# Kernel tuning notes

Hardware: AMD Instinct MI355X
Metric: run time of the kernel (lower is better)

## Reference

```python
import jax, jax.numpy as jnp
import numpy as np

B, H, N, D, RPE = 2, 8, 4096, 64, 64
LAYERS = 3


def _rms(x):
    # SimpleRMSNorm: x / sqrt(mean(x^2) + eps), no learned scale
    return x / jnp.sqrt(jnp.mean(x * x, axis=-1, keepdims=True) + 1e-8)


def setup_inputs() -> dict:
    key = jax.random.key(0)
    ks = jax.random.split(key, 7)
    s = 1.0 / np.sqrt(RPE)
    return {
        "x": jax.random.normal(ks[0], (B, H, N, D), dtype=jnp.float32),
        "w_in": jax.random.normal(ks[1], (1, RPE), dtype=jnp.float32) * 0.5,
        "b_in": jax.random.normal(ks[2], (RPE,), dtype=jnp.float32) * 0.02,
        "w_hid": jax.random.normal(ks[3], (LAYERS, RPE, RPE), dtype=jnp.float32) * s,
        "b_hid": jax.random.normal(ks[4], (LAYERS, RPE), dtype=jnp.float32) * 0.02,
        "w_out": jax.random.normal(ks[5], (RPE, H * D), dtype=jnp.float32) * s,
        "b_out": jax.random.normal(ks[6], (H * D,), dtype=jnp.float32) * 0.02,
    }


def reference(x, w_in, b_in, w_hid, b_hid, w_out, b_out):
    n = x.shape[-2]
    dt = x.dtype

    def rpe(idx):  # idx: (m, 1) relative-position features
        h = idx @ w_in + b_in  # (m, RPE)
        for i in range(LAYERS):  # non-residual: x = layer(x)
            h = jax.nn.relu(_rms(h)) @ w_hid[i] + b_hid[i]
        h = jax.nn.relu(_rms(h)) @ w_out + b_out  # (m, H*D)
        return h.reshape(-1, H, D).transpose(1, 0, 2)  # (H, m, D)

    zero_idx = jnp.ones((1, 1), dt)
    pos_idx = (1.0 / jnp.arange(2, n + 1, dtype=dt)).reshape(n - 1, 1)
    neg_idx = (-1.0 / jnp.arange(n, 1, -1, dtype=dt)).reshape(n - 1, 1)

    zero_k = rpe(zero_idx)  # (H, 1, D); used for both T[0] slots like the torch code
    a = jnp.concatenate([zero_k, rpe(pos_idx), zero_k, rpe(neg_idx)], axis=1)  # (H, 2n, D)
    # act_type='none' -> identity activation on a

    # Toeplitz matvec as circular conv of length 2n via FFT
    y = jnp.fft.rfft(x, 2 * n, axis=-2)          # (B, H, n+1, D) complex
    v = jnp.fft.rfft(a, 2 * n, axis=-2)[None]    # (1, H, n+1, D) complex
    out = jnp.fft.irfft(v * y, 2 * n, axis=-2)[:, :, :n, :]
    return out.astype(dt)
```

## Files before the change

### kernel.cpp

```cpp
#include <hip/hip_runtime.h>

#define N_SEQ 4096
#define N_FFT 8192
#define LAYERS 3
#define FT 512
#define PIDX(i) ((i) + ((i) >> 5))

template<int M>
__device__ inline void pass16_fwd(float* re, float* im, int tid)
{
    const int Q = M >> 4;
    const int j = tid & (Q - 1);
    const int G = tid / Q;
    const int base = G * M + j;
    const float KR[4] = {1.f, 0.9238795325f, 0.7071067812f, 0.3826834324f};
    const float KI[4] = {0.f, -0.3826834324f, -0.7071067812f, -0.9238795325f};
    float xr[4][4], xi[4][4];
#pragma unroll
    for (int a = 0; a < 4; ++a)
#pragma unroll
        for (int b = 0; b < 4; ++b) {
            int idx = PIDX(base + a * (M >> 2) + b * Q);
            xr[a][b] = re[idx]; xi[a][b] = im[idx];
        }
    float cj, sj;
    __sincosf(-6.283185307179586f / (float)M * (float)j, &sj, &cj);
#pragma unroll
    for (int b = 0; b < 4; ++b) {
        float c1 = cj * KR[b] - sj * KI[b];
        float s1 = cj * KI[b] + sj * KR[b];
        float c2 = c1 * c1 - s1 * s1, s2 = 2.f * c1 * s1;
        float c3 = c2 * c1 - s2 * s1, s3 = c2 * s1 + s2 * c1;
        float ar = xr[0][b] + xr[2][b], ai = xi[0][b] + xi[2][b];
        float br = xr[0][b] - xr[2][b], bi = xi[0][b] - xi[2][b];
        float cr = xr[1][b] + xr[3][b], ci = xi[1][b] + xi[3][b];
        float dr = xi[1][b] - xi[3][b], di = -(xr[1][b] - xr[3][b]);
        xr[0][b] = ar + cr;               xi[0][b] = ai + ci;
        float t1r = br + dr, t1i = bi + di;
        xr[1][b] = t1r * c1 - t1i * s1;   xi[1][b] = t1r * s1 + t1i * c1;
        float t2r = ar - cr, t2i = ai - ci;
        xr[2][b] = t2r * c2 - t2i * s2;   xi[2][b] = t2r * s2 + t2i * c2;
        float t3r = br - dr, t3i = bi - di;
        xr[3][b] = t3r * c3 - t3i * s3;   xi[3][b] = t3r * s3 + t3i * c3;
    }
    {
        float e1c = cj * cj - sj * sj, e1s = 2.f * cj * sj;
        float c1 = e1c * e1c - e1s * e1s, s1 = 2.f * e1c * e1s;
        float c2 = c1 * c1 - s1 * s1, s2 = 2.f * c1 * s1;
        float c3 = c2 * c1 - s2 * s1, s3 = c2 * s1 + s2 * c1;
#pragma unroll
        for (int a = 0; a < 4; ++a) {
            float ar = xr[a][0] + xr[a][2], ai = xi[a][0] + xi[a][2];
            float br = xr[a][0] - xr[a][2], bi = xi[a][0] - xi[a][2];
            float cr = xr[a][1] + xr[a][3], ci = xi[a][1] + xi[a][3];
            float dr = xi[a][1] - xi[a][3], di = -(xr[a][1] - xr[a][3]);
            xr[a][0] = ar + cr;               xi[a][0] = ai + ci;
            float t1r = br + dr, t1i = bi + di;
            xr[a][1] = t1r * c1 - t1i * s1;   xi[a][1] = t1r * s1 + t1i * c1;
            float t2r = ar - cr, t2i = ai - ci;
            xr[a][2] = t2r * c2 - t2i * s2;   xi[a][2] = t2r * s2 + t2i * c2;
            float t3r = br - dr, t3i = bi - di;
            xr[a][3] = t3r * c3 - t3i * s3;   xi[a][3] = t3r * s3 + t3i * c3;
        }
    }
#pragma unroll
    for (int a = 0; a < 4; ++a)
#pragma unroll
        for (int b = 0; b < 4; ++b) {
            int idx = PIDX(base + a * (M >> 2) + b * Q);
            re[idx] = xr[a][b]; im[idx] = xi[a][b];
        }
}

template<int M>
__device__ inline void pass16_inv(float* re, float* im, int tid)
{
    const int Q = M >> 4;
    const int j = tid & (Q - 1);
    const int G = tid / Q;
    const int base = G * M + j;
    const float KR[4] = {1.f, 0.9238795325f, 0.7071067812f, 0.3826834324f};
    const float KI[4] = {0.f, 0.3826834324f, 0.7071067812f, 0.9238795325f};
    float xr[4][4], xi[4][4];
#pragma unroll
    for (int a = 0; a < 4; ++a)
#pragma unroll
        for (int b = 0; b < 4; ++b) {
            int idx = PIDX(base + a * (M >> 2) + b * Q);
            xr[a][b] = re[idx]; xi[a][b] = im[idx];
        }
    float cj, sj;
    __sincosf(6.283185307179586f / (float)M * (float)j, &sj, &cj);
    {
        float e1c = cj * cj - sj * sj, e1s = 2.f * cj * sj;
        float c1 = e1c * e1c - e1s * e1s, s1 = 2.f * e1c * e1s;
        float c2 = c1 * c1 - s1 * s1, s2 = 2.f * c1 * s1;
        float c3 = c2 * c1 - s2 * s1, s3 = c2 * s1 + s2 * c1;
#pragma unroll
        for (int a = 0; a < 4; ++a) {
            float t0r = xr[a][0], t0i = xi[a][0];
            float t1r = xr[a][1] * c1 - xi[a][1] * s1, t1i = xr[a][1] * s1 + xi[a][1] * c1;
            float t2r = xr[a][2] * c2 - xi[a][2] * s2, t2i = xr[a][2] * s2 + xi[a][2] * c2;
            float t3r = xr[a][3] * c3 - xi[a][3] * s3, t3i = xr[a][3] * s3 + xi[a][3] * c3;
            float pr = t0r + t2r, pi = t0i + t2i;
            float qr = t0r - t2r, qi = t0i - t2i;
            float rr = t1r + t3r, ri = t1i + t3i;
            float sr = -(t1i - t3i), si = t1r - t3r;
            xr[a][0] = pr + rr; xi[a][0] = pi + ri;
            xr[a][1] = qr + sr; xi[a][1] = qi + si;
            xr[a][2] = pr - rr; xi[a][2] = pi - ri;
            xr[a][3] = qr - sr; xi[a][3] = qi - si;
        }
    }
#pragma unroll
    for (int b = 0; b < 4; ++b) {
        float c1 = cj * KR[b] - sj * KI[b];
        float s1 = cj * KI[b] + sj * KR[b];
        float c2 = c1 * c1 - s1 * s1, s2 = 2.f * c1 * s1;
        float c3 = c2 * c1 - s2 * s1, s3 = c2 * s1 + s2 * c1;
        float t0r = xr[0][b], t0i = xi[0][b];
        float t1r = xr[1][b] * c1 - xi[1][b] * s1, t1i = xr[1][b] * s1 + xi[1][b] * c1;
        float t2r = xr[2][b] * c2 - xi[2][b] * s2, t2i = xr[2][b] * s2 + xi[2][b] * c2;
        float t3r = xr[3][b] * c3 - xi[3][b] * s3, t3i = xr[3][b] * s3 + xi[3][b] * c3;
        float pr = t0r + t2r, pi = t0i + t2i;
        float qr = t0r - t2r, qi = t0i - t2i;
        float rr = t1r + t3r, ri = t1i + t3i;
        float sr = -(t1i - t3i), si = t1r - t3r;
        xr[0][b] = pr + rr; xi[0][b] = pi + ri;
        xr[1][b] = qr + sr; xi[1][b] = qi + si;
        xr[2][b] = pr - rr; xi[2][b] = pi - ri;
        xr[3][b] = qr - sr; xi[3][b] = qi - si;
    }
#pragma unroll
    for (int a = 0; a < 4; ++a)
#pragma unroll
        for (int b = 0; b < 4; ++b) {
            int idx = PIDX(base + a * (M >> 2) + b * Q);
            re[idx] = xr[a][b]; im[idx] = xi[a][b];
        }
}

__device__ inline void fwd8(float* zr, float* zi, int o)
{
    const float R = 0.70710678118654752f;
    {
        float ar = zr[o] + zr[o+4], ai = zi[o] + zi[o+4];
        float br = zr[o] - zr[o+4], bi = zi[o] - zi[o+4];
        float cr = zr[o+2] + zr[o+6], ci = zi[o+2] + zi[o+6];
        float dr = zi[o+2] - zi[o+6], di = -(zr[o+2] - zr[o+6]);
        zr[o]   = ar + cr; zi[o]   = ai + ci;
        zr[o+2] = br + dr; zi[o+2] = bi + di;
        zr[o+4] = ar - cr; zi[o+4] = ai - ci;
        zr[o+6] = br - dr; zi[o+6] = bi - di;
    }
    {
        float ar = zr[o+1] + zr[o+5], ai = zi[o+1] + zi[o+5];
        float br = zr[o+1] - zr[o+5], bi = zi[o+1] - zi[o+5];
        float cr = zr[o+3] + zr[o+7], ci = zi[o+3] + zi[o+7];
        float dr = zi[o+3] - zi[o+7], di = -(zr[o+3] - zr[o+7]);
        zr[o+1] = ar + cr; zi[o+1] = ai + ci;
        float t1r = br + dr, t1i = bi + di;
        zr[o+3] = R * (t1r + t1i); zi[o+3] = R * (t1i - t1r);
        float t2r = ar - cr, t2i = ai - ci;
        zr[o+5] = t2i;  zi[o+5] = -t2r;
        float t3r = br - dr, t3i = bi - di;
        zr[o+7] = R * (t3i - t3r); zi[o+7] = -R * (t3r + t3i);
    }
#pragma unroll
    for (int p = 0; p < 8; p += 2) {
        float ur = zr[o+p], ui = zi[o+p], vr = zr[o+p+1], vi = zi[o+p+1];
        zr[o+p]   = ur + vr; zi[o+p]   = ui + vi;
        zr[o+p+1] = ur - vr; zi[o+p+1] = ui - vi;
    }
}

__device__ inline void inv8(float* zr, float* zi, int o)
{
    const float R = 0.70710678118654752f;
#pragma unroll
    for (int p = 0; p < 8; p += 2) {
        float ur = zr[o+p], ui = zi[o+p], vr = zr[o+p+1], vi = zi[o+p+1];
        zr[o+p]   = ur + vr; zi[o+p]   = ui + vi;
        zr[o+p+1] = ur - vr; zi[o+p+1] = ui - vi;
    }
    {
        float t0r = zr[o],   t0i = zi[o];
        float t1r = zr[o+2], t1i = zi[o+2];
        float t2r = zr[o+4], t2i = zi[o+4];
        float t3r = zr[o+6], t3i = zi[o+6];
        float pr = t0r + t2r, pi = t0i + t2i;
        float qr = t0r - t2r, qi = t0i - t2i;
        float rr = t1r + t3r, ri = t1i + t3i;
        float sr = -(t1i - t3i), si = t1r - t3r;
        zr[o]   = pr + rr; zi[o]   = pi + ri;
        zr[o+2] = qr + sr; zi[o+2] = qi + si;
        zr[o+4] = pr - rr; zi[o+4] = pi - ri;
        zr[o+6] = qr - sr; zi[o+6] = qi - si;
    }
    {
        float t0r = zr[o+1], t0i = zi[o+1];
        float yr = zr[o+3], yi = zi[o+3];
        float t1r = R * (yr - yi), t1i = R * (yr + yi);
        yr = zr[o+5]; yi = zi[o+5];
        float t2r = -yi, t2i = yr;
        yr = zr[o+7]; yi = zi[o+7];
        float t3r = -R * (yr + yi), t3i = R * (yr - yi);
        float pr = t0r + t2r, pi = t0i + t2i;
        float qr = t0r - t2r, qi = t0i - t2i;
        float rr = t1r + t3r, ri = t1i + t3i;
        float sr = -(t1i - t3i), si = t1r - t3r;
        zr[o+1] = pr + rr; zi[o+1] = pi + ri;
        zr[o+3] = qr + sr; zi[o+3] = qi + si;
        zr[o+5] = pr - rr; zi[o+5] = pi - ri;
        zr[o+7] = qr - sr; zi[o+7] = qi - si;
    }
}

__global__ __launch_bounds__(512) void prep_kernel(
    const float* __restrict__ x,
    const float* __restrict__ w_in, const float* __restrict__ b_in,
    const float* __restrict__ w_hid, const float* __restrict__ b_hid,
    const float* __restrict__ w_out, const float* __restrict__ b_out,
    float* __restrict__ a_t, float2* __restrict__ xt2)
{
    __shared__ __align__(16) char smem[35328];
    const int tid = threadIdx.x;

    if (blockIdx.x >= 128) {
        float (*t0)[65] = (float (*)[65])smem;
        float (*t1)[65] = (float (*)[65])(smem + 16640);
        int bb = blockIdx.x - 128;
        int h = bb >> 6;
        int nb = bb & 63;
        int lx = tid & 63;
        int ly = tid >> 6;
        const float* s0 = x + ((size_t)h * N_SEQ + nb * 64) * 64;
        const float* s1 = x + ((size_t)(8 + h) * N_SEQ + nb * 64) * 64;
        for (int r = ly; r < 64; r += 8) {
            t0[r][lx] = s0[r * 64 + lx];
            t1[r][lx] = s1[r * 64 + lx];
        }
        __syncthreads();
        for (int r = ly; r < 64; r += 8) {
            float2* dst = xt2 + (size_t)(h * 64 + r) * N_SEQ + nb * 64;
            dst[lx] = make_float2(t0[lx][r], t1[lx][r]);
        }
        return;
    }

    float4* wl        = (float4*)smem;
    float (*ubuf)[65] = (float (*)[65])(smem + 16384);
    float (*sums)[9]  = (float (*)[9])(smem + 33024);
    const int p   = tid & 63;
    const int oct = tid >> 6;
    const int pos = blockIdx.x * 64 + p;

    float v;
    if (pos == 0 || pos == N_SEQ) v = 1.0f;
    else if (pos < N_SEQ)         v = 1.0f / (float)(pos + 1);
    else                          v = -1.0f / (float)(2 * N_SEQ + 1 - pos);

    float h[8];
#pragma unroll
    for (int i = 0; i < 8; ++i) {
        int f = oct * 8 + i;
        h[i] = v * w_in[f] + b_in[f];
    }
    for (int L = 0; L < LAYERS; ++L) {
        const float4* wsrc = (const float4*)(w_hid + L * 4096);
        wl[tid] = wsrc[tid];
        wl[tid + 512] = wsrc[tid + 512];
        float s = 0.f;
#pragma unroll
        for (int i = 0; i < 8; ++i) s += h[i] * h[i];
        sums[p][oct] = s;
        __syncthreads();
        float tot = 0.f;
#pragma unroll
        for (int g = 0; g < 8; ++g) tot += sums[p][g];
        float r = rsqrtf(tot * (1.f / 64.f) + 1e-8f);
#pragma unroll
        for (int i = 0; i < 8; ++i)
            ubuf[p][oct * 8 + i] = fmaxf(h[i] * r, 0.f);
        __syncthreads();
        float acc[8];
#pragma unroll
        for (int i = 0; i < 8; ++i) acc[i] = b_hid[L * 64 + oct * 8 + i];
#pragma unroll 4
        for (int j = 0; j < 64; ++j) {
            float uj = ubuf[p][j];
            float4 w0 = wl[j * 16 + oct * 2];
            float4 w1 = wl[j * 16 + oct * 2 + 1];
            acc[0] = fmaf(uj, w0.x, acc[0]); acc[1] = fmaf(uj, w0.y, acc[1]);
            acc[2] = fmaf(uj, w0.z, acc[2]); acc[3] = fmaf(uj, w0.w, acc[3]);
            acc[4] = fmaf(uj, w1.x, acc[4]); acc[5] = fmaf(uj, w1.y, acc[5]);
            acc[6] = fmaf(uj, w1.z, acc[6]); acc[7] = fmaf(uj, w1.w, acc[7]);
        }
#pragma unroll
        for (int i = 0; i < 8; ++i) h[i] = acc[i];
        __syncthreads();
    }
    {
        float s = 0.f;
#pragma unroll
        for (int i = 0; i < 8; ++i) s += h[i] * h[i];
        sums[p][oct] = s;
        __syncthreads();
        float tot = 0.f;
#pragma unroll
        for (int g = 0; g < 8; ++g) tot += sums[p][g];
        float r = rsqrtf(tot * (1.f / 64.f) + 1e-8f);
#pragma unroll
        for (int i = 0; i < 8; ++i)
            ubuf[p][oct * 8 + i] = fmaxf(h[i] * r, 0.f);
        __syncthreads();
    }
    for (int c = 0; c < 8; ++c) {
        float4 wreg0, wreg1;
        {
            int i4 = tid;
            wreg0 = *(const float4*)(w_out + (i4 >> 4) * 512 + c * 64 + (i4 & 15) * 4);
            i4 = tid + 512;
            wreg1 = *(const float4*)(w_out + (i4 >> 4) * 512 + c * 64 + (i4 & 15) * 4);
        }
        __syncthreads();
        wl[tid] = wreg0;
        wl[tid + 512] = wreg1;
        __syncthreads();
        float acc[8];
#pragma unroll
        for (int i = 0; i < 8; ++i) acc[i] = b_out[c * 64 + oct * 8 + i];
#pragma unroll 4
        for (int j = 0; j < 64; ++j) {
            float uj = ubuf[p][j];
            float4 w0 = wl[j * 16 + oct * 2];
            float4 w1 = wl[j * 16 + oct * 2 + 1];
            acc[0] = fmaf(uj, w0.x, acc[0]); acc[1] = fmaf(uj, w0.y, acc[1]);
            acc[2] = fmaf(uj, w0.z, acc[2]); acc[3] = fmaf(uj, w0.w, acc[3]);
            acc[4] = fmaf(uj, w1.x, acc[4]); acc[5] = fmaf(uj, w1.y, acc[5]);
            acc[6] = fmaf(uj, w1.z, acc[6]); acc[7] = fmaf(uj, w1.w, acc[7]);
        }
#pragma unroll
        for (int i = 0; i < 8; ++i)
            a_t[(size_t)(c * 64 + oct * 8 + i) * N_FFT + pos] = acc[i];
    }
}

__global__ __launch_bounds__(FT, 2) void conv_kernel(const float* __restrict__ a_t,
                                                     const float2* __restrict__ xt2,
                                                     float2* __restrict__ out_t2)
{
    __shared__ float re[8448];
    __shared__ float im[8448];
    const int tid = threadIdx.x;
    const int hd = blockIdx.x;
    const float JR = 0.9238795325f;
    const float JI = -0.3826834324f;

    {
        const float* src = a_t + (size_t)hd * N_FFT;
        float ck, sk;
        __sincosf(-6.283185307179586f / 8192.f * (float)tid, &sk, &ck);
#pragma unroll
        for (int pp = 0; pp < 4; ++pp) {
            int k = pp * FT + tid;
            float x0 = src[k], x1 = src[k + 2048], x2 = src[k + 4096], x3 = src[k + 6144];
            float ar = x0 + x2, br = x0 - x2;
            float cr = x1 + x3, e = x1 - x3;
            re[PIDX(k)] = ar + cr; im[PIDX(k)] = 0.f;
            float c1 = ck, s1 = sk;
            float c2 = c1 * c1 - s1 * s1, s2 = 2.f * c1 * s1;
            float c3 = c2 * c1 - s2 * s1, s3 = c2 * s1 + s2 * c1;
            re[PIDX(k + 2048)] = br * c1 + e * s1;  im[PIDX(k + 2048)] = br * s1 - e * c1;
            float t2r = ar - cr;
            re[PIDX(k + 4096)] = t2r * c2;          im[PIDX(k + 4096)] = t2r * s2;
            re[PIDX(k + 6144)] = br * c3 - e * s3;  im[PIDX(k + 6144)] = br * s3 + e * c3;
            float tc = ck * JR - sk * JI; sk = ck * JI + sk * JR; ck = tc;
        }
    }
    __syncthreads();
    pass16_fwd<2048>(re, im, tid);
    __syncthreads();
    pass16_fwd<128>(re, im, tid);
    __syncthreads();
    float afr[16], afi[16];
    {
        const int base = tid * 16;
#pragma unroll
        for (int c = 0; c < 16; ++c) { int idx = PIDX(base + c); afr[c] = re[idx]; afi[c] = im[idx]; }
        fwd8(afr, afi, 0); fwd8(afr, afi, 8);
    }
    __syncthreads();
    {
        const float2* src = xt2 + (size_t)hd * N_SEQ;
        float ck, sk;
        __sincosf(-6.283185307179586f / 8192.f * (float)tid, &sk, &ck);
#pragma unroll
        for (int pp = 0; pp < 4; ++pp) {
            int k = pp * FT + tid;
            float2 z0 = src[k], z1 = src[k + 2048];
            float ar = z0.x, ai = z0.y;
            float cr = z1.x, ci = z1.y;
            float dr = z1.y, di = -z1.x;
            re[PIDX(k)] = ar + cr; im[PIDX(k)] = ai + ci;
            float c1 = ck, s1 = sk;
            float c2 = c1 * c1 - s1 * s1, s2 = 2.f * c1 * s1;
            float c3 = c2 * c1 - s2 * s1, s3 = c2 * s1 + s2 * c1;
            float t1r = ar + dr, t1i = ai + di;
            re[PIDX(k + 2048)] = t1r * c1 - t1i * s1; im[PIDX(k + 2048)] = t1r * s1 + t1i * c1;
            float t2r = ar - cr, t2i = ai - ci;
            re[PIDX(k + 4096)] = t2r * c2 - t2i * s2; im[PIDX(k + 4096)] = t2r * s2 + t2i * c2;
            float t3r = ar - dr, t3i = ai - di;
            re[PIDX(k + 6144)] = t3r * c3 - t3i * s3; im[PIDX(k + 6144)] = t3r * s3 + t3i * c3;
            float tc = ck * JR - sk * JI; sk = ck * JI + sk * JR; ck = tc;
        }
    }
    __syncthreads();
    pass16_fwd<2048>(re, im, tid);
    __syncthreads();
    pass16_fwd<128>(re, im, tid);
    __syncthreads();
    {
        const int base = tid * 16;
        float zr[16], zi[16];
#pragma unroll
        for (int c = 0; c < 16; ++c) { int idx = PIDX(base + c); zr[c] = re[idx]; zi[c] = im[idx]; }
        fwd8(zr, zi, 0); fwd8(zr, zi, 8);
        const float inv = 1.0f / (float)N_FFT;
#pragma unroll
        for (int c = 0; c < 16; ++c) {
            float xr = zr[c], xi_ = zi[c];
            zr[c] = (xr * afr[c] - xi_ * afi[c]) * inv;
            zi[c] = (xr * afi[c] + xi_ * afr[c]) * inv;
        }
        inv8(zr, zi, 0); inv8(zr, zi, 8);
#pragma unroll
        for (int c = 0; c < 16; ++c) { int idx = PIDX(base + c); re[idx] = zr[c]; im[idx] = zi[c]; }
    }
    __syncthreads();
    pass16_inv<128>(re, im, tid);
    __syncthreads();
    pass16_inv<2048>(re, im, tid);
    __syncthreads();
    {
        float2* dst = out_t2 + (size_t)hd * N_SEQ;
        float ck, sk;
        __sincosf(6.283185307179586f / 8192.f * (float)tid, &sk, &ck);
        const float JcR = 0.9238795325f, JcI = 0.3826834324f;
#pragma unroll
        for (int pp = 0; pp < 4; ++pp) {
            int k = pp * FT + tid;
            float c1 = ck, s1 = sk;
            float c2 = c1 * c1 - s1 * s1, s2 = 2.f * c1 * s1;
            float c3 = c2 * c1 - s2 * s1, s3 = c2 * s1 + s2 * c1;
            float t0r = re[PIDX(k)],        t0i = im[PIDX(k)];
            float y1r = re[PIDX(k + 2048)], y1i = im[PIDX(k + 2048)];
            float y2r = re[PIDX(k + 4096)], y2i = im[PIDX(k + 4096)];
            float y3r = re[PIDX(k + 6144)], y3i = im[PIDX(k + 6144)];
            float t1r = y1r * c1 - y1i * s1, t1i = y1r * s1 + y1i * c1;
            float t2r = y2r * c2 - y2i * s2, t2i = y2r * s2 + y2i * c2;
            float t3r = y3r * c3 - y3i * s3, t3i = y3r * s3 + y3i * c3;
            float pr = t0r + t2r, pi = t0i + t2i;
            float qr = t0r - t2r, qi = t0i - t2i;
            float rr = t1r + t3r, ri = t1i + t3i;
            float sr = -(t1i - t3i), si = t1r - t3r;
            dst[k]        = make_float2(pr + rr, pi + ri);
            dst[k + 2048] = make_float2(qr + sr, qi + si);
            float tc = ck * JcR - sk * JcI; sk = ck * JcI + sk * JcR; ck = tc;
        }
    }
}

__global__ __launch_bounds__(256) void transpose_o_kernel(const float2* __restrict__ out_t2,
                                                          float* __restrict__ out)
{
    __shared__ float t0[64][65];
    __shared__ float t1[64][65];
    int h = blockIdx.x >> 6;
    int nb = blockIdx.x & 63;
    int lx = threadIdx.x & 63;
    int ly = threadIdx.x >> 6;
    for (int r = ly; r < 64; r += 4) {
        float2 v = out_t2[(size_t)(h * 64 + r) * N_SEQ + nb * 64 + lx];
        t0[r][lx] = v.x;
        t1[r][lx] = v.y;
    }
    __syncthreads();
    float* d0 = out + ((size_t)h * N_SEQ + nb * 64) * 64;
    float* d1 = out + ((size_t)(8 + h) * N_SEQ + nb * 64) * 64;
    for (int r = ly; r < 64; r += 4) {
        d0[r * 64 + lx] = t0[lx][r];
        d1[r * 64 + lx] = t1[lx][r];
    }
}

extern "C" void kernel_launch(void* const* d_in, const int* in_sizes, int n_in,
                              void* d_out, int out_size, void* d_ws, size_t ws_size,
                              hipStream_t stream)
{
    const float* x     = (const float*)d_in[0];
    const float* w_in  = (const float*)d_in[1];
    const float* b_in  = (const float*)d_in[2];
    const float* w_hid = (const float*)d_in[3];
    const float* b_hid = (const float*)d_in[4];
    const float* w_out = (const float*)d_in[5];
    const float* b_out = (const float*)d_in[6];
    float* out = (float*)d_out;

    char* ws = (char*)d_ws;
    float2* xt2    = (float2*)ws;
    float*  a_t    = (float*)(ws + (size_t)16 * 1024 * 1024);
    float2* out_t2 = (float2*)(ws + (size_t)32 * 1024 * 1024);

    prep_kernel<<<640, 512, 0, stream>>>(x, w_in, b_in, w_hid, b_hid, w_out, b_out,
                                         a_t, xt2);
    conv_kernel<<<512, FT, 0, stream>>>(a_t, xt2, out_t2);
    transpose_o_kernel<<<512, 256, 0, stream>>>(out_t2, out);
}
```

Measured before the change: 151.1 us.

## Retile RPE MLP prep: 32 positions per block with register-tiled output GEMM

The RPE MLP portion of prep_kernel now handles 32 positions per block instead of 64, so it runs on 256 blocks rather than 128. Each thread covers 4 hidden features per position. The final 64x512 output projection becomes a register-blocked 8x4 tile per thread, with w_out staged in shared memory in 16-row chunks. This cuts the eight serial weight reloads and raises FMA reuse per shared-memory load. In exchange it uses more shared memory and registers, and the a_t stores are now strided per thread.

```diff
diff --git a/kernel.cpp b/kernel.cpp
--- a/kernel.cpp
+++ b/kernel.cpp
@@ -216,20 +216,20 @@
     }
 }
 
-__global__ __launch_bounds__(512) void prep_kernel(
+__global__ __launch_bounds__(512, 4) void prep_kernel(
     const float* __restrict__ x,
     const float* __restrict__ w_in, const float* __restrict__ b_in,
     const float* __restrict__ w_hid, const float* __restrict__ b_hid,
     const float* __restrict__ w_out, const float* __restrict__ b_out,
     float* __restrict__ a_t, float2* __restrict__ xt2)
 {
-    __shared__ __align__(16) char smem[35328];
+    __shared__ __align__(16) char smem[43264];
     const int tid = threadIdx.x;
 
-    if (blockIdx.x >= 128) {
+    if (blockIdx.x >= 256) {
         float (*t0)[65] = (float (*)[65])smem;
         float (*t1)[65] = (float (*)[65])(smem + 16640);
-        int bb = blockIdx.x - 128;
+        int bb = blockIdx.x - 256;
         int h = bb >> 6;
         int nb = bb & 63;
         int lx = tid & 63;
@@ -248,101 +248,129 @@
         return;
     }
 
-    float4* wl        = (float4*)smem;
-    float (*ubuf)[65] = (float (*)[65])(smem + 16384);
-    float (*sums)[9]  = (float (*)[9])(smem + 33024);
-    const int p   = tid & 63;
-    const int oct = tid >> 6;
-    const int pos = blockIdx.x * 64 + p;
-
-    float v;
-    if (pos == 0 || pos == N_SEQ) v = 1.0f;
-    else if (pos < N_SEQ)         v = 1.0f / (float)(pos + 1);
-    else                          v = -1.0f / (float)(2 * N_SEQ + 1 - pos);
-
-    float h[8];
-#pragma unroll
-    for (int i = 0; i < 8; ++i) {
-        int f = oct * 8 + i;
-        h[i] = v * w_in[f] + b_in[f];
-    }
-    for (int L = 0; L < LAYERS; ++L) {
-        const float4* wsrc = (const float4*)(w_hid + L * 4096);
-        wl[tid] = wsrc[tid];
-        wl[tid + 512] = wsrc[tid + 512];
-        float s = 0.f;
-#pragma unroll
-        for (int i = 0; i < 8; ++i) s += h[i] * h[i];
-        sums[p][oct] = s;
+    float (*ubuf)[65] = (float (*)[65])smem;
+    float (*sums)[17] = (float (*)[17])(smem + 8320);
+    float4* wl        = (float4*)(smem + 10496);
+
+    {
+        const int p = tid & 31;
+        const int s = tid >> 5;
+        const int pos = blockIdx.x * 32 + p;
+        float v;
+        if (pos == 0 || pos == N_SEQ) v = 1.0f;
+        else if (pos < N_SEQ)         v = 1.0f / (float)(pos + 1);
+        else                          v = -1.0f / (float)(2 * N_SEQ + 1 - pos);
+
+        float h[4];
+#pragma unroll
+        for (int i = 0; i < 4; ++i) {
+            int f = s * 4 + i;
+            h[i] = v * w_in[f] + b_in[f];
+        }
+        for (int L = 0; L < LAYERS; ++L) {
+            const float4* wsrc = (const float4*)(w_hid + L * 4096);
+            wl[tid] = wsrc[tid];
+            wl[tid + 512] = wsrc[tid + 512];
+            float s2 = h[0]*h[0] + h[1]*h[1] + h[2]*h[2] + h[3]*h[3];
+            sums[p][s] = s2;
+            __syncthreads();
+            float tot = 0.f;
+#pragma unroll
+            for (int g = 0; g < 16; ++g) tot += sums[p][g];
+            float r = rsqrtf(tot * (1.f / 64.f) + 1e-8f);
+#pragma unroll
+            for (int i = 0; i < 4; ++i)
+                ubuf[p][s * 4 + i] = fmaxf(h[i] * r, 0.f);
+            __syncthreads();
+            float acc[4];
+#pragma unroll
+            for (int i = 0; i < 4; ++i) acc[i] = b_hid[L * 64 + s * 4 + i];
+#pragma unroll 8
+            for (int j = 0; j < 64; ++j) {
+                float uj = ubuf[p][j];
+                float4 w = wl[j * 16 + s];
+                acc[0] = fmaf(uj, w.x, acc[0]); acc[1] = fmaf(uj, w.y, acc[1]);
+                acc[2] = fmaf(uj, w.z, acc[2]); acc[3] = fmaf(uj, w.w, acc[3]);
+            }
+#pragma unroll
+            for (int i = 0; i < 4; ++i) h[i] = acc[i];
+            __syncthreads();
+        }
+        float s2 = h[0]*h[0] + h[1]*h[1] + h[2]*h[2] + h[3]*h[3];
+        sums[p][s] = s2;
         __syncthreads();
         float tot = 0.f;
 #pragma unroll
-        for (int g = 0; g < 8; ++g) tot += sums[p][g];
+        for (int g = 0; g < 16; ++g) tot += sums[p][g];
         float r = rsqrtf(tot * (1.f / 64.f) + 1e-8f);
 #pragma unroll
-        for (int i = 0; i < 8; ++i)
-            ubuf[p][oct * 8 + i] = fmaxf(h[i] * r, 0.f);
+        for (int i = 0; i < 4; ++i)
+            ubuf[p][s * 4 + i] = fmaxf(h[i] * r, 0.f);
         __syncthreads();
-        float acc[8];
-#pragma unroll
-        for (int i = 0; i < 8; ++i) acc[i] = b_hid[L * 64 + oct * 8 + i];
-#pragma unroll 4
-        for (int j = 0; j < 64; ++j) {
-            float uj = ubuf[p][j];
-            float4 w0 = wl[j * 16 + oct * 2];
-            float4 w1 = wl[j * 16 + oct * 2 + 1];
-            acc[0] = fmaf(uj, w0.x, acc[0]); acc[1] = fmaf(uj, w0.y, acc[1]);
-            acc[2] = fmaf(uj, w0.z, acc[2]); acc[3] = fmaf(uj, w0.w, acc[3]);
-            acc[4] = fmaf(uj, w1.x, acc[4]); acc[5] = fmaf(uj, w1.y, acc[5]);
-            acc[6] = fmaf(uj, w1.z, acc[6]); acc[7] = fmaf(uj, w1.w, acc[7]);
-        }
-#pragma unroll
-        for (int i = 0; i < 8; ++i) h[i] = acc[i];
-        __syncthreads();
-    }
-    {
-        float s = 0.f;
-#pragma unroll
-        for (int i = 0; i < 8; ++i) s += h[i] * h[i];
-        sums[p][oct] = s;
-        __syncthreads();
-        float tot = 0.f;
-#pragma unroll
-        for (int g = 0; g < 8; ++g) tot += sums[p][g];
-        float r = rsqrtf(tot * (1.f / 64.f) + 1e-8f);
-#pragma unroll
-        for (int i = 0; i < 8; ++i)
-            ubuf[p][oct * 8 + i] = fmaxf(h[i] * r, 0.f);
-        __syncthreads();
-    }
-    for (int c = 0; c < 8; ++c) {
-        float4 wreg0, wreg1;
-        {
-            int i4 = tid;
-            wreg0 = *(const float4*)(w_out + (i4 >> 4) * 512 + c * 64 + (i4 & 15) * 4);
-            i4 = tid + 512;
-            wreg1 = *(const float4*)(w_out + (i4 >> 4) * 512 + c * 64 + (i4 & 15) * 4);
-        }
-        __syncthreads();
-        wl[tid] = wreg0;
-        wl[tid + 512] = wreg1;
-        __syncthreads();
-        float acc[8];
-#pragma unroll
-        for (int i = 0; i < 8; ++i) acc[i] = b_out[c * 64 + oct * 8 + i];
-#pragma unroll 4
-        for (int j = 0; j < 64; ++j) {
-            float uj = ubuf[p][j];
-            float4 w0 = wl[j * 16 + oct * 2];
-            float4 w1 = wl[j * 16 + oct * 2 + 1];
-            acc[0] = fmaf(uj, w0.x, acc[0]); acc[1] = fmaf(uj, w0.y, acc[1]);
-            acc[2] = fmaf(uj, w0.z, acc[2]); acc[3] = fmaf(uj, w0.w, acc[3]);
-            acc[4] = fmaf(uj, w1.x, acc[4]); acc[5] = fmaf(uj, w1.y, acc[5]);
-            acc[6] = fmaf(uj, w1.z, acc[6]); acc[7] = fmaf(uj, w1.w, acc[7]);
-        }
-#pragma unroll
-        for (int i = 0; i < 8; ++i)
-            a_t[(size_t)(c * 64 + oct * 8 + i) * N_FFT + pos] = acc[i];
+    }
+
+    {
+        const int o  = tid >> 3;
+        const int pg = tid & 7;
+        const int pos0 = blockIdx.x * 32;
+        float4* wt = wl;
+        float acc[8][4];
+#pragma unroll
+        for (int ii = 0; ii < 8; ++ii) {
+            float bo = b_out[o * 8 + ii];
+#pragma unroll
+            for (int i = 0; i < 4; ++i) acc[ii][i] = bo;
+        }
+        for (int jc = 0; jc < 4; ++jc) {
+            float4 wreg[4];
+#pragma unroll
+            for (int k = 0; k < 4; ++k) {
+                int i4 = k * 512 + tid;
+                int jj = i4 >> 7, f4 = i4 & 127;
+                wreg[k] = *(const float4*)(w_out + (jc * 16 + jj) * 512 + f4 * 4);
+            }
+            __syncthreads();
+#pragma unroll
+            for (int k = 0; k < 4; ++k) {
+                int i4 = k * 512 + tid;
+                wt[i4] = wreg[k];
+            }
+            __syncthreads();
+#pragma unroll
+            for (int jj = 0; jj < 16; ++jj) {
+                int j = jc * 16 + jj;
+                float4 w0 = wt[jj * 128 + o * 2];
+                float4 w1 = wt[jj * 128 + o * 2 + 1];
+                float u0 = ubuf[pg * 4 + 0][j];
+                float u1 = ubuf[pg * 4 + 1][j];
+                float u2 = ubuf[pg * 4 + 2][j];
+                float u3 = ubuf[pg * 4 + 3][j];
+                acc[0][0] = fmaf(u0, w0.x, acc[0][0]); acc[0][1] = fmaf(u1, w0.x, acc[0][1]);
+                acc[0][2] = fmaf(u2, w0.x, acc[0][2]); acc[0][3] = fmaf(u3, w0.x, acc[0][3]);
+                acc[1][0] = fmaf(u0, w0.y, acc[1][0]); acc[1][1] = fmaf(u1, w0.y, acc[1][1]);
+                acc[1][2] = fmaf(u2, w0.y, acc[1][2]); acc[1][3] = fmaf(u3, w0.y, acc[1][3]);
+                acc[2][0] = fmaf(u0, w0.z, acc[2][0]); acc[2][1] = fmaf(u1, w0.z, acc[2][1]);
+                acc[2][2] = fmaf(u2, w0.z, acc[2][2]); acc[2][3] = fmaf(u3, w0.z, acc[2][3]);
+                acc[3][0] = fmaf(u0, w0.w, acc[3][0]); acc[3][1] = fmaf(u1, w0.w, acc[3][1]);
+                acc[3][2] = fmaf(u2, w0.w, acc[3][2]); acc[3][3] = fmaf(u3, w0.w, acc[3][3]);
+                acc[4][0] = fmaf(u0, w1.x, acc[4][0]); acc[4][1] = fmaf(u1, w1.x, acc[4][1]);
+                acc[4][2] = fmaf(u2, w1.x, acc[4][2]); acc[4][3] = fmaf(u3, w1.x, acc[4][3]);
+                acc[5][0] = fmaf(u0, w1.y, acc[5][0]); acc[5][1] = fmaf(u1, w1.y, acc[5][1]);
+                acc[5][2] = fmaf(u2, w1.y, acc[5][2]); acc[5][3] = fmaf(u3, w1.y, acc[5][3]);
+                acc[6][0] = fmaf(u0, w1.z, acc[6][0]); acc[6][1] = fmaf(u1, w1.z, acc[6][1]);
+                acc[6][2] = fmaf(u2, w1.z, acc[6][2]); acc[6][3] = fmaf(u3, w1.z, acc[6][3]);
+                acc[7][0] = fmaf(u0, w1.w, acc[7][0]); acc[7][1] = fmaf(u1, w1.w, acc[7][1]);
+                acc[7][2] = fmaf(u2, w1.w, acc[7][2]); acc[7][3] = fmaf(u3, w1.w, acc[7][3]);
+            }
+            __syncthreads();
+        }
+#pragma unroll
+        for (int ii = 0; ii < 8; ++ii) {
+            int f = o * 8 + ii;
+#pragma unroll
+            for (int i = 0; i < 4; ++i)
+                a_t[(size_t)f * N_FFT + pos0 + pg * 4 + i] = acc[ii][i];
+        }
     }
 }
 
@@ -512,7 +540,7 @@
     float*  a_t    = (float*)(ws + (size_t)16 * 1024 * 1024);
     float2* out_t2 = (float2*)(ws + (size_t)32 * 1024 * 1024);
 
-    prep_kernel<<<640, 512, 0, stream>>>(x, w_in, b_in, w_hid, b_hid, w_out, b_out,
+    prep_kernel<<<768, 512, 0, stream>>>(x, w_in, b_in, w_hid, b_hid, w_out, b_out,
                                          a_t, xt2);
     conv_kernel<<<512, FT, 0, stream>>>(a_t, xt2, out_t2);
     transpose_o_kernel<<<512, 256, 0, stream>>>(out_t2, out);
```

Result: faster. 144.2 us (-4.6%).

## Read MLP weights via wave-uniform scalar loads instead of LDS staging

Applied to the files above, without the earlier changes.

The prep kernel no longer stages hidden and output weights in shared memory. Each wave's index is made wave-uniform with readfirstlane, so weight rows can be fetched with scalar loads straight from global memory. The output layer now has each wave compute a full 64-column chunk in 64 register accumulators, which removes the 8-chunk loop and its barriers. The aim is fewer LDS round-trips and syncs, and smaller shared memory allowing more blocks per CU, at the cost of higher register pressure and scalar-cache traffic.

```diff
diff --git a/kernel.cpp b/kernel.cpp
--- a/kernel.cpp
+++ b/kernel.cpp
@@ -216,14 +216,14 @@
     }
 }
 
-__global__ __launch_bounds__(512) void prep_kernel(
+__global__ __launch_bounds__(512, 4) void prep_kernel(
     const float* __restrict__ x,
     const float* __restrict__ w_in, const float* __restrict__ b_in,
     const float* __restrict__ w_hid, const float* __restrict__ b_hid,
     const float* __restrict__ w_out, const float* __restrict__ b_out,
     float* __restrict__ a_t, float2* __restrict__ xt2)
 {
-    __shared__ __align__(16) char smem[35328];
+    __shared__ __align__(16) char smem[33536];
     const int tid = threadIdx.x;
 
     if (blockIdx.x >= 128) {
@@ -248,11 +248,10 @@
         return;
     }
 
-    float4* wl        = (float4*)smem;
-    float (*ubuf)[65] = (float (*)[65])(smem + 16384);
-    float (*sums)[9]  = (float (*)[9])(smem + 33024);
-    const int p   = tid & 63;
-    const int oct = tid >> 6;
+    float (*ubuf)[65] = (float (*)[65])smem;
+    float (*sums)[9]  = (float (*)[9])(smem + 16640);
+    const int p = tid & 63;
+    const int w = __builtin_amdgcn_readfirstlane(tid >> 6);
     const int pos = blockIdx.x * 64 + p;
 
     float v;
@@ -263,17 +262,14 @@
     float h[8];
 #pragma unroll
     for (int i = 0; i < 8; ++i) {
-        int f = oct * 8 + i;
+        int f = w * 8 + i;
         h[i] = v * w_in[f] + b_in[f];
     }
     for (int L = 0; L < LAYERS; ++L) {
-        const float4* wsrc = (const float4*)(w_hid + L * 4096);
-        wl[tid] = wsrc[tid];
-        wl[tid + 512] = wsrc[tid + 512];
         float s = 0.f;
 #pragma unroll
         for (int i = 0; i < 8; ++i) s += h[i] * h[i];
-        sums[p][oct] = s;
+        sums[p][w] = s;
         __syncthreads();
         float tot = 0.f;
 #pragma unroll
@@ -281,30 +277,28 @@
         float r = rsqrtf(tot * (1.f / 64.f) + 1e-8f);
 #pragma unroll
         for (int i = 0; i < 8; ++i)
-            ubuf[p][oct * 8 + i] = fmaxf(h[i] * r, 0.f);
+            ubuf[p][w * 8 + i] = fmaxf(h[i] * r, 0.f);
         __syncthreads();
         float acc[8];
-#pragma unroll
-        for (int i = 0; i < 8; ++i) acc[i] = b_hid[L * 64 + oct * 8 + i];
-#pragma unroll 4
+        const float* bh = b_hid + L * 64 + w * 8;
+#pragma unroll
+        for (int i = 0; i < 8; ++i) acc[i] = bh[i];
+        const float* wbase = w_hid + L * 4096 + w * 8;
         for (int j = 0; j < 64; ++j) {
             float uj = ubuf[p][j];
-            float4 w0 = wl[j * 16 + oct * 2];
-            float4 w1 = wl[j * 16 + oct * 2 + 1];
-            acc[0] = fmaf(uj, w0.x, acc[0]); acc[1] = fmaf(uj, w0.y, acc[1]);
-            acc[2] = fmaf(uj, w0.z, acc[2]); acc[3] = fmaf(uj, w0.w, acc[3]);
-            acc[4] = fmaf(uj, w1.x, acc[4]); acc[5] = fmaf(uj, w1.y, acc[5]);
-            acc[6] = fmaf(uj, w1.z, acc[6]); acc[7] = fmaf(uj, w1.w, acc[7]);
+            const float* wr = wbase + j * 64;
+#pragma unroll
+            for (int i = 0; i < 8; ++i)
+                acc[i] = fmaf(uj, wr[i], acc[i]);
         }
 #pragma unroll
         for (int i = 0; i < 8; ++i) h[i] = acc[i];
-        __syncthreads();
     }
     {
         float s = 0.f;
 #pragma unroll
         for (int i = 0; i < 8; ++i) s += h[i] * h[i];
-        sums[p][oct] = s;
+        sums[p][w] = s;
         __syncthreads();
         float tot = 0.f;
 #pragma unroll
@@ -312,37 +306,27 @@
         float r = rsqrtf(tot * (1.f / 64.f) + 1e-8f);
 #pragma unroll
         for (int i = 0; i < 8; ++i)
-            ubuf[p][oct * 8 + i] = fmaxf(h[i] * r, 0.f);
+            ubuf[p][w * 8 + i] = fmaxf(h[i] * r, 0.f);
         __syncthreads();
     }
-    for (int c = 0; c < 8; ++c) {
-        float4 wreg0, wreg1;
-        {
-            int i4 = tid;
-            wreg0 = *(const float4*)(w_out + (i4 >> 4) * 512 + c * 64 + (i4 & 15) * 4);
-            i4 = tid + 512;
-            wreg1 = *(const float4*)(w_out + (i4 >> 4) * 512 + c * 64 + (i4 & 15) * 4);
-        }
-        __syncthreads();
-        wl[tid] = wreg0;
-        wl[tid + 512] = wreg1;
-        __syncthreads();
-        float acc[8];
-#pragma unroll
-        for (int i = 0; i < 8; ++i) acc[i] = b_out[c * 64 + oct * 8 + i];
-#pragma unroll 4
+    {
+        const int c = w;
+        float acc[64];
+        const float* bo = b_out + c * 64;
+#pragma unroll
+        for (int f = 0; f < 64; ++f) acc[f] = bo[f];
+        const float* wbase = w_out + c * 64;
         for (int j = 0; j < 64; ++j) {
             float uj = ubuf[p][j];
-            float4 w0 = wl[j * 16 + oct * 2];
-            float4 w1 = wl[j * 16 + oct * 2 + 1];
-            acc[0] = fmaf(uj, w0.x, acc[0]); acc[1] = fmaf(uj, w0.y, acc[1]);
-            acc[2] = fmaf(uj, w0.z, acc[2]); acc[3] = fmaf(uj, w0.w, acc[3]);
-            acc[4] = fmaf(uj, w1.x, acc[4]); acc[5] = fmaf(uj, w1.y, acc[5]);
-            acc[6] = fmaf(uj, w1.z, acc[6]); acc[7] = fmaf(uj, w1.w, acc[7]);
-        }
-#pragma unroll
-        for (int i = 0; i < 8; ++i)
-            a_t[(size_t)(c * 64 + oct * 8 + i) * N_FFT + pos] = acc[i];
+            const float* wr = wbase + j * 512;
+#pragma unroll
+            for (int f = 0; f < 64; ++f)
+                acc[f] = fmaf(uj, wr[f], acc[f]);
+        }
+        float* dst = a_t + pos;
+#pragma unroll
+        for (int f = 0; f < 64; ++f)
+            dst[(size_t)(c * 64 + f) * N_FFT] = acc[f];
     }
 }
 
```

New measurement: 160.6 us. 6.3% more time.
